# Kernel tuning notes

Measured on AMD Instinct MI355X. Metric: run time of the kernel, lower is better.

## Reference

```python
import jax, jax.numpy as jnp
import numpy as np

B, LS, LH, D1, D2 = 16, 1024, 1024, 1024, 1024


def setup_inputs() -> dict:
    key = jax.random.key(0)
    k1, k2, k3 = jax.random.split(key, 3)
    S = jax.random.normal(k1, (B, LS, D1), dtype=jnp.float32)
    H = jax.random.normal(k2, (B, LH, D2), dtype=jnp.float32)
    pad_mask = jnp.zeros((B, LS, LH), dtype=jnp.float32)  # additive mask
    W_w = jax.random.normal(k3, (D2, D1), dtype=jnp.float32) / np.sqrt(D1)
    W_b = jnp.zeros((D2,), dtype=jnp.float32)
    return {"S": S, "H": H, "pad_mask": pad_mask, "W_w": W_w, "W_b": W_b}


def reference(S, H, pad_mask, W_w, W_b):
    # Linear projection: S_ = S @ W^T + b  -> [B, LS, D2]
    S_ = jnp.einsum('bsd,ed->bse', S, W_w) + W_b
    # Unscaled dot-product scores: [B, LS, LH]
    score = jnp.einsum('bse,bte->bst', S_, H)
    score = score + pad_mask  # additive pad mask
    score = jax.nn.softmax(score, axis=-1)
    # Weighted sum of H: [B, LS, D2]
    out = jnp.einsum('bst,bte->bse', score, H)
    return out
```

## Files before the change

### kernel.cpp

```cpp
#include <hip/hip_runtime.h>
#include <stdint.h>

typedef _Float16 half8 __attribute__((ext_vector_type(8)));
typedef float floatx4 __attribute__((ext_vector_type(4)));

__device__ __forceinline__ uint16_t f16bits(_Float16 h) {
  union { _Float16 f; uint16_t u; } x; x.f = h; return x.u;
}

__device__ __forceinline__ void g2l16(const void* g, void* l) {
  __builtin_amdgcn_global_load_lds((const __attribute__((address_space(1))) void*)g,
                                   (__attribute__((address_space(3))) void*)l,
                                   16, 0, 0);
}

__global__ __launch_bounds__(256) void split_f16_kernel(
    const float* __restrict__ x, uint16_t* __restrict__ hi,
    uint16_t* __restrict__ lo, int n4) {
  int i = blockIdx.x * 256 + threadIdx.x;
  if (i >= n4) return;
  float4 v = ((const float4*)x)[i];
  ushort4 h, l;
  _Float16 a;
  a = (_Float16)v.x; h.x = f16bits(a); l.x = f16bits((_Float16)(v.x - (float)a));
  a = (_Float16)v.y; h.y = f16bits(a); l.y = f16bits((_Float16)(v.y - (float)a));
  a = (_Float16)v.z; h.z = f16bits(a); l.z = f16bits((_Float16)(v.z - (float)a));
  a = (_Float16)v.w; h.w = f16bits(a); l.w = f16bits((_Float16)(v.w - (float)a));
  ((ushort4*)hi)[i] = h;
  ((ushort4*)lo)[i] = l;
}

__global__ __launch_bounds__(256) void split_h_kernel(
    const float* __restrict__ src, uint16_t* __restrict__ hi,
    uint16_t* __restrict__ lo, uint16_t* __restrict__ ht) {
  __shared__ uint16_t tile[64][65];
  const int e0 = blockIdx.x * 64;
  const int t0 = blockIdx.y * 64;
  const size_t bb = (size_t)blockIdx.z << 20;
  const int r = threadIdx.x >> 4;
  const int c = (threadIdx.x & 15) * 4;
#pragma unroll
  for (int it = 0; it < 4; ++it) {
    const int tr = r + it * 16;
    const size_t idx = bb + (size_t)(t0 + tr) * 1024 + e0 + c;
    float4 v = *(const float4*)(src + idx);
    ushort4 h, l;
    _Float16 a;
    a = (_Float16)v.x; h.x = f16bits(a); l.x = f16bits((_Float16)(v.x - (float)a));
    a = (_Float16)v.y; h.y = f16bits(a); l.y = f16bits((_Float16)(v.y - (float)a));
    a = (_Float16)v.z; h.z = f16bits(a); l.z = f16bits((_Float16)(v.z - (float)a));
    a = (_Float16)v.w; h.w = f16bits(a); l.w = f16bits((_Float16)(v.w - (float)a));
    *(ushort4*)(hi + idx) = h;
    *(ushort4*)(lo + idx) = l;
    tile[c + 0][tr] = h.x;
    tile[c + 1][tr] = h.y;
    tile[c + 2][tr] = h.z;
    tile[c + 3][tr] = h.w;
  }
  __syncthreads();
#pragma unroll
  for (int it = 0; it < 4; ++it) {
    const int er = r + it * 16;
    ushort4 o;
    o.x = tile[er][c + 0];
    o.y = tile[er][c + 1];
    o.z = tile[er][c + 2];
    o.w = tile[er][c + 3];
    *(ushort4*)(ht + bb + (size_t)(e0 + er) * 1024 + t0 + c) = o;
  }
}

template <bool SPLIT, int MODE, int GMAP>
__global__ __launch_bounds__(512, 2) void gemm_bt(
    const uint16_t* __restrict__ Ahi, const uint16_t* __restrict__ Alo,
    const uint16_t* __restrict__ Bhi, const uint16_t* __restrict__ Blo,
    uint16_t* __restrict__ Chi, uint16_t* __restrict__ Clo,
    float* __restrict__ Cf, const float* __restrict__ mask,
    const float* __restrict__ bias, int N, int K,
    long batchA, long batchB, long batchC) {
  constexpr int NBUF = SPLIT ? 2 : 1;
  __shared__ __align__(16) uint16_t sA[2][NBUF][256 * 32];
  __shared__ __align__(16) uint16_t sB[2][NBUF][256 * 32];

  const int tid = threadIdx.x;
  const int lane = tid & 63;
  const int w = tid >> 6;
  const int wr = w >> 2, wc = w & 3;
  const int quad = lane >> 4, l16 = lane & 15;

  int m_t, n_t, z;
  if constexpr (GMAP == 0) {
    m_t = blockIdx.x; n_t = blockIdx.y; z = 0;
  } else {
    z = blockIdx.x; m_t = blockIdx.y >> 2; n_t = blockIdx.y & 3;
  }
  const int m0 = m_t * 256;
  const int n0 = n_t * 256;
  const size_t zA = (size_t)z * batchA;
  const size_t zB = (size_t)z * batchB;
  const size_t zC = (size_t)z * batchC;

  const int r0 = w * 32 + (lane >> 2);
  const int ldc = (((lane & 3) ^ ((lane >> 2) & 3)) * 16);
  const size_t rowskip = (size_t)16 * K * 2;

  const char* gAh = (const char*)(Ahi + zA + (size_t)(m0 + r0) * K) + ldc;
  const char* gBh = (const char*)(Bhi + zB + (size_t)(n0 + r0) * K) + ldc;
  const char* gAl = gAh;
  const char* gBl = gBh;
  if constexpr (SPLIT) {
    gAl = (const char*)(Alo + zA + (size_t)(m0 + r0) * K) + ldc;
    gBl = (const char*)(Blo + zB + (size_t)(n0 + r0) * K) + ldc;
  }

  auto stage = [&](int buf, int kb) {
    g2l16(gAh + kb, &sA[buf][0][(w * 32) * 32]);
    g2l16(gAh + rowskip + kb, &sA[buf][0][(w * 32 + 16) * 32]);
    g2l16(gBh + kb, &sB[buf][0][(w * 32) * 32]);
    g2l16(gBh + rowskip + kb, &sB[buf][0][(w * 32 + 16) * 32]);
    if constexpr (SPLIT) {
      g2l16(gAl + kb, &sA[buf][NBUF - 1][(w * 32) * 32]);
      g2l16(gAl + rowskip + kb, &sA[buf][NBUF - 1][(w * 32 + 16) * 32]);
      g2l16(gBl + kb, &sB[buf][NBUF - 1][(w * 32) * 32]);
      g2l16(gBl + rowskip + kb, &sB[buf][NBUF - 1][(w * 32 + 16) * 32]);
    }
  };

  const int aoff = (wr * 128 + l16) * 32 + ((quad ^ (l16 & 3)) * 8);
  const int boff = (wc * 64 + l16) * 32 + ((quad ^ (l16 & 3)) * 8);

  floatx4 acc[8][4];
  floatx4 zero = {0.f, 0.f, 0.f, 0.f};
#pragma unroll
  for (int i = 0; i < 8; ++i)
#pragma unroll
    for (int j = 0; j < 4; ++j) acc[i][j] = zero;

  const int nkt = K >> 5;
  stage(0, 0);
  __syncthreads();
  int cur = 0;
  for (int kt = 0; kt < nkt; ++kt) {
    if (kt + 1 < nkt) stage(cur ^ 1, (kt + 1) * 64);

    const uint16_t* pAh = &sA[cur][0][0];
    const uint16_t* pBh = &sB[cur][0][0];
    const uint16_t* pAl = &sA[cur][NBUF - 1][0];
    const uint16_t* pBl = &sB[cur][NBUF - 1][0];
    half8 fbh[4], fbl[4];
    if constexpr (SPLIT) {
#pragma unroll
      for (int j = 0; j < 4; ++j) fbl[j] = *(const half8*)&pBl[boff + j * 512];
    }
#pragma unroll
    for (int j = 0; j < 4; ++j) fbh[j] = *(const half8*)&pBh[boff + j * 512];
    __builtin_amdgcn_s_setprio(1);
#pragma unroll
    for (int i = 0; i < 8; ++i) {
      half8 fah = *(const half8*)&pAh[aoff + i * 512];
      if constexpr (SPLIT) {
        half8 fal = *(const half8*)&pAl[aoff + i * 512];
#pragma unroll
        for (int j = 0; j < 4; ++j)
          acc[i][j] = __builtin_amdgcn_mfma_f32_16x16x32_f16(fah, fbl[j], acc[i][j], 0, 0, 0);
#pragma unroll
        for (int j = 0; j < 4; ++j)
          acc[i][j] = __builtin_amdgcn_mfma_f32_16x16x32_f16(fah, fbh[j], acc[i][j], 0, 0, 0);
#pragma unroll
        for (int j = 0; j < 4; ++j)
          acc[i][j] = __builtin_amdgcn_mfma_f32_16x16x32_f16(fal, fbh[j], acc[i][j], 0, 0, 0);
      } else {
#pragma unroll
        for (int j = 0; j < 4; ++j)
          acc[i][j] = __builtin_amdgcn_mfma_f32_16x16x32_f16(fah, fbh[j], acc[i][j], 0, 0, 0);
      }
    }
    __builtin_amdgcn_s_setprio(0);
    __syncthreads();
    cur ^= 1;
  }

  const int crow0 = m0 + wr * 128 + quad * 4;
  const int ccol0 = n0 + wc * 64 + l16;
#pragma unroll
  for (int j = 0; j < 4; ++j) {
    const int col = ccol0 + j * 16;
    float bj = 0.f;
    if constexpr (MODE == 0) bj = bias[col];
#pragma unroll
    for (int i = 0; i < 8; ++i) {
#pragma unroll
      for (int r = 0; r < 4; ++r) {
        const int row = crow0 + i * 16 + r;
        const size_t idx = zC + (size_t)row * N + col;
        float v = acc[i][j][r];
        if constexpr (MODE == 0) {
          v += bj;
          _Float16 h = (_Float16)v;
          Chi[idx] = f16bits(h);
          Clo[idx] = f16bits((_Float16)(v - (float)h));
        } else if constexpr (MODE == 1) {
          Cf[idx] = v + mask[idx];
        } else {
          Cf[idx] = v;
        }
      }
    }
  }
}

__global__ __launch_bounds__(256) void softmax_kernel(
    const float* __restrict__ sc, uint16_t* __restrict__ p) {
  const int row = blockIdx.x;
  const float* x = sc + (size_t)row * 1024;
  const int t = threadIdx.x;
  float4 v = ((const float4*)x)[t];
  float m = fmaxf(fmaxf(v.x, v.y), fmaxf(v.z, v.w));
#pragma unroll
  for (int off = 32; off; off >>= 1) m = fmaxf(m, __shfl_xor(m, off));
  __shared__ float redm[4];
  __shared__ float reds[4];
  const int wv = t >> 6, ln = t & 63;
  if (ln == 0) redm[wv] = m;
  __syncthreads();
  m = fmaxf(fmaxf(redm[0], redm[1]), fmaxf(redm[2], redm[3]));
  float e0 = __expf(v.x - m), e1 = __expf(v.y - m);
  float e2 = __expf(v.z - m), e3 = __expf(v.w - m);
  float s = e0 + e1 + e2 + e3;
#pragma unroll
  for (int off = 32; off; off >>= 1) s += __shfl_xor(s, off);
  if (ln == 0) reds[wv] = s;
  __syncthreads();
  s = reds[0] + reds[1] + reds[2] + reds[3];
  float inv = 1.f / s;
  ushort4 o;
  o.x = f16bits((_Float16)(e0 * inv));
  o.y = f16bits((_Float16)(e1 * inv));
  o.z = f16bits((_Float16)(e2 * inv));
  o.w = f16bits((_Float16)(e3 * inv));
  ((ushort4*)(p + (size_t)row * 1024))[t] = o;
}

__global__ __launch_bounds__(256) void transpose_f16_kernel(
    const float* __restrict__ src, uint16_t* __restrict__ dst) {
  __shared__ uint16_t tile[64][65];
  const int e0 = blockIdx.x * 64;
  const int t0 = blockIdx.y * 64;
  const size_t bb = (size_t)blockIdx.z << 20;
  const int r = threadIdx.x >> 4;
  const int c = (threadIdx.x & 15) * 4;
#pragma unroll
  for (int it = 0; it < 4; ++it) {
    const int tr = r + it * 16;
    float4 v = *(const float4*)(src + bb + (size_t)(t0 + tr) * 1024 + e0 + c);
    tile[c + 0][tr] = f16bits((_Float16)v.x);
    tile[c + 1][tr] = f16bits((_Float16)v.y);
    tile[c + 2][tr] = f16bits((_Float16)v.z);
    tile[c + 3][tr] = f16bits((_Float16)v.w);
  }
  __syncthreads();
#pragma unroll
  for (int it = 0; it < 4; ++it) {
    const int er = r + it * 16;
    ushort4 o;
    o.x = tile[er][c + 0];
    o.y = tile[er][c + 1];
    o.z = tile[er][c + 2];
    o.w = tile[er][c + 3];
    *(ushort4*)(dst + bb + (size_t)(e0 + er) * 1024 + t0 + c) = o;
  }
}

extern "C" void kernel_launch(void* const* d_in, const int* in_sizes, int n_in,
                              void* d_out, int out_size, void* d_ws, size_t ws_size,
                              hipStream_t stream) {
  (void)in_sizes; (void)n_in; (void)out_size;
  const float* S    = (const float*)d_in[0];
  const float* H    = (const float*)d_in[1];
  const float* mask = (const float*)d_in[2];
  const float* Ww   = (const float*)d_in[3];
  const float* Wb   = (const float*)d_in[4];
  float* out = (float*)d_out;
  char* ws = (char*)d_ws;
  const size_t MB = 1024ull * 1024ull;

  uint16_t* Whi  = (uint16_t*)(ws + 0 * MB);
  uint16_t* Wlo  = (uint16_t*)(ws + 2 * MB);
  uint16_t* Pjhi = (uint16_t*)(ws + 4 * MB);
  uint16_t* Pjlo = (uint16_t*)(ws + 36 * MB);
  uint16_t* Hhi  = (uint16_t*)(ws + 68 * MB);
  uint16_t* Hlo  = (uint16_t*)(ws + 100 * MB);
  uint16_t* Shi  = (uint16_t*)(ws + 132 * MB);
  uint16_t* Slo  = (uint16_t*)(ws + 164 * MB);
  float*    SC   = (float*)(ws + 132 * MB);
  uint16_t* PR   = (uint16_t*)(ws + 68 * MB);

  const bool roomy = ws_size >= 229ull * MB;
  uint16_t* HT = roomy ? (uint16_t*)(ws + 196 * MB)
                       : (uint16_t*)(ws + 100 * MB);

  split_f16_kernel<<<16384, 256, 0, stream>>>(S, Shi, Slo, 4 * 1024 * 1024);
  split_f16_kernel<<<1024, 256, 0, stream>>>(Ww, Whi, Wlo, 256 * 1024);
  if (roomy) {
    split_h_kernel<<<dim3(16, 16, 16), 256, 0, stream>>>(H, Hhi, Hlo, HT);
  } else {
    split_f16_kernel<<<16384, 256, 0, stream>>>(H, Hhi, Hlo, 4 * 1024 * 1024);
  }

  gemm_bt<true, 0, 0><<<dim3(64, 4, 1), 512, 0, stream>>>(
      Shi, Slo, Whi, Wlo, Pjhi, Pjlo, nullptr, nullptr, Wb,
      1024, 1024, 0, 0, 0);
  gemm_bt<true, 1, 1><<<dim3(16, 16, 1), 512, 0, stream>>>(
      Pjhi, Pjlo, Hhi, Hlo, nullptr, nullptr, SC, mask, nullptr,
      1024, 1024, 1048576, 1048576, 1048576);
  softmax_kernel<<<16384, 256, 0, stream>>>(SC, PR);
  if (!roomy) {
    transpose_f16_kernel<<<dim3(16, 16, 16), 256, 0, stream>>>(H, HT);
  }
  gemm_bt<false, 2, 1><<<dim3(16, 16, 1), 512, 0, stream>>>(
      PR, nullptr, HT, nullptr, nullptr, nullptr, out, nullptr, nullptr,
      1024, 1024, 1048576, 1048576, 1048576);
}
```

Before: 556.4 us.

## Replace double-buffered GEMM staging with five-slot half-tile LDS ring pipeline

Replaces the two-stage LDS double buffer in the split-f16 GEMM with a five-slot ring of half-tile units. Loads are issued deeper ahead, interleaved across four sub-phases of the MFMA loop, and guarded by explicit vmcnt waits and raw s_barriers instead of a full __syncthreads per k-step. The aim is to hide global-to-LDS latency and spread barrier stalls. In exchange it adds more LDS per block, which may reduce occupancy, more barriers per iteration, and hand-tuned waitcnt logic that is fragile.

```diff
diff --git a/kernel.cpp b/kernel.cpp
--- a/kernel.cpp
+++ b/kernel.cpp
@@ -78,9 +78,11 @@
     float* __restrict__ Cf, const float* __restrict__ mask,
     const float* __restrict__ bias, int N, int K,
     long batchA, long batchB, long batchC) {
-  constexpr int NBUF = SPLIT ? 2 : 1;
-  __shared__ __align__(16) uint16_t sA[2][NBUF][256 * 32];
-  __shared__ __align__(16) uint16_t sB[2][NBUF][256 * 32];
+  constexpr int UNIT = SPLIT ? 16384 : 8192;
+  constexpr int OAL = 4096;
+  constexpr int OBH = SPLIT ? 8192 : 4096;
+  constexpr int OBL = 12288;
+  __shared__ __align__(16) uint16_t lds[5 * UNIT];
 
   const int tid = threadIdx.x;
   const int lane = tid & 63;
@@ -100,34 +102,31 @@
   const size_t zB = (size_t)z * batchB;
   const size_t zC = (size_t)z * batchC;
 
-  const int r0 = w * 32 + (lane >> 2);
+  const int r4 = w * 16 + (lane >> 2);
   const int ldc = (((lane & 3) ^ ((lane >> 2) & 3)) * 16);
-  const size_t rowskip = (size_t)16 * K * 2;
-
-  const char* gAh = (const char*)(Ahi + zA + (size_t)(m0 + r0) * K) + ldc;
-  const char* gBh = (const char*)(Bhi + zB + (size_t)(n0 + r0) * K) + ldc;
+  const size_t halfskip = (size_t)128 * K * 2;
+
+  const char* gAh = (const char*)(Ahi + zA + (size_t)(m0 + r4) * K) + ldc;
+  const char* gBh = (const char*)(Bhi + zB + (size_t)(n0 + r4) * K) + ldc;
   const char* gAl = gAh;
   const char* gBl = gBh;
   if constexpr (SPLIT) {
-    gAl = (const char*)(Alo + zA + (size_t)(m0 + r0) * K) + ldc;
-    gBl = (const char*)(Blo + zB + (size_t)(n0 + r0) * K) + ldc;
-  }
-
-  auto stage = [&](int buf, int kb) {
-    g2l16(gAh + kb, &sA[buf][0][(w * 32) * 32]);
-    g2l16(gAh + rowskip + kb, &sA[buf][0][(w * 32 + 16) * 32]);
-    g2l16(gBh + kb, &sB[buf][0][(w * 32) * 32]);
-    g2l16(gBh + rowskip + kb, &sB[buf][0][(w * 32 + 16) * 32]);
-    if constexpr (SPLIT) {
-      g2l16(gAl + kb, &sA[buf][NBUF - 1][(w * 32) * 32]);
-      g2l16(gAl + rowskip + kb, &sA[buf][NBUF - 1][(w * 32 + 16) * 32]);
-      g2l16(gBl + kb, &sB[buf][NBUF - 1][(w * 32) * 32]);
-      g2l16(gBl + rowskip + kb, &sB[buf][NBUF - 1][(w * 32 + 16) * 32]);
-    }
+    gAl = (const char*)(Alo + zA + (size_t)(m0 + r4) * K) + ldc;
+    gBl = (const char*)(Blo + zB + (size_t)(n0 + r4) * K) + ldc;
+  }
+
+  auto issue_unit = [&](int u, int sl) {
+    const int tt = u >> 1;
+    const size_t go = (size_t)(u & 1) * halfskip + (size_t)tt * 64;
+    uint16_t* ub = &lds[sl * UNIT] + w * 512;
+    g2l16(gAh + go, ub);
+    if constexpr (SPLIT) g2l16(gAl + go, ub + OAL);
+    g2l16(gBh + go, ub + OBH);
+    if constexpr (SPLIT) g2l16(gBl + go, ub + OBL);
   };
 
-  const int aoff = (wr * 128 + l16) * 32 + ((quad ^ (l16 & 3)) * 8);
-  const int boff = (wc * 64 + l16) * 32 + ((quad ^ (l16 & 3)) * 8);
+  const int aoff = l16 * 32 + ((quad ^ (l16 & 3)) * 8);
+  const int boff = ((wc & 1) * 64 + l16) * 32 + ((quad ^ (l16 & 3)) * 8);
 
   floatx4 acc[8][4];
   floatx4 zero = {0.f, 0.f, 0.f, 0.f};
@@ -137,47 +136,89 @@
     for (int j = 0; j < 4; ++j) acc[i][j] = zero;
 
   const int nkt = K >> 5;
-  stage(0, 0);
-  __syncthreads();
-  int cur = 0;
-  for (int kt = 0; kt < nkt; ++kt) {
-    if (kt + 1 < nkt) stage(cur ^ 1, (kt + 1) * 64);
-
-    const uint16_t* pAh = &sA[cur][0][0];
-    const uint16_t* pBh = &sB[cur][0][0];
-    const uint16_t* pAl = &sA[cur][NBUF - 1][0];
-    const uint16_t* pBl = &sB[cur][NBUF - 1][0];
+  const int NU = nkt * 2;
+
+  issue_unit(0, 0);
+  issue_unit(1, 1);
+  issue_unit(2, 2);
+  if constexpr (SPLIT)
+    asm volatile("s_waitcnt vmcnt(4)" ::: "memory");
+  else
+    asm volatile("s_waitcnt vmcnt(2)" ::: "memory");
+  __builtin_amdgcn_s_barrier();
+  asm volatile("" ::: "memory");
+
+  int sl0 = 0;
+  for (int t = 0; t < nkt; ++t) {
+    const int sl1 = (sl0 + 1 == 5) ? 0 : sl0 + 1;
+    const int si0 = (sl0 + 3 >= 5) ? sl0 - 2 : sl0 + 3;
+    const int si1 = (sl0 + 4 >= 5) ? sl0 - 1 : sl0 + 4;
+    const uint16_t* uA = &lds[(wr ? sl1 : sl0) * UNIT];
+    const uint16_t* uB = &lds[((wc >> 1) ? sl1 : sl0) * UNIT];
     half8 fbh[4], fbl[4];
-    if constexpr (SPLIT) {
-#pragma unroll
-      for (int j = 0; j < 4; ++j) fbl[j] = *(const half8*)&pBl[boff + j * 512];
+#pragma unroll
+    for (int p = 0; p < 4; ++p) {
+      half8 fah[2], fal[2];
+      if (p == 0) {
+        if constexpr (SPLIT) {
+#pragma unroll
+          for (int j = 0; j < 4; ++j)
+            fbl[j] = *(const half8*)&uB[OBL + boff + j * 512];
+        }
+#pragma unroll
+        for (int j = 0; j < 4; ++j)
+          fbh[j] = *(const half8*)&uB[OBH + boff + j * 512];
+      }
+      fah[0] = *(const half8*)&uA[aoff + (2 * p) * 512];
+      fah[1] = *(const half8*)&uA[aoff + (2 * p + 1) * 512];
+      if constexpr (SPLIT) {
+        fal[0] = *(const half8*)&uA[OAL + aoff + (2 * p) * 512];
+        fal[1] = *(const half8*)&uA[OAL + aoff + (2 * p + 1) * 512];
+      }
+      if (p == 0 && 2 * t + 3 < NU) issue_unit(2 * t + 3, si0);
+      if (p == 2 && 2 * t + 4 < NU) issue_unit(2 * t + 4, si1);
+      asm volatile("" ::: "memory");
+      __builtin_amdgcn_s_barrier();
+      asm volatile("s_waitcnt lgkmcnt(0)" ::: "memory");
+      __builtin_amdgcn_sched_barrier(0);
+      __builtin_amdgcn_s_setprio(1);
+#pragma unroll
+      for (int ii = 0; ii < 2; ++ii) {
+        const int i = 2 * p + ii;
+        if constexpr (SPLIT) {
+#pragma unroll
+          for (int j = 0; j < 4; ++j)
+            acc[i][j] = __builtin_amdgcn_mfma_f32_16x16x32_f16(fah[ii], fbl[j], acc[i][j], 0, 0, 0);
+#pragma unroll
+          for (int j = 0; j < 4; ++j)
+            acc[i][j] = __builtin_amdgcn_mfma_f32_16x16x32_f16(fah[ii], fbh[j], acc[i][j], 0, 0, 0);
+#pragma unroll
+          for (int j = 0; j < 4; ++j)
+            acc[i][j] = __builtin_amdgcn_mfma_f32_16x16x32_f16(fal[ii], fbh[j], acc[i][j], 0, 0, 0);
+        } else {
+#pragma unroll
+          for (int j = 0; j < 4; ++j)
+            acc[i][j] = __builtin_amdgcn_mfma_f32_16x16x32_f16(fah[ii], fbh[j], acc[i][j], 0, 0, 0);
+        }
+      }
+      __builtin_amdgcn_s_setprio(0);
+      if (p < 3) {
+        asm volatile("" ::: "memory");
+        __builtin_amdgcn_s_barrier();
+      }
     }
-#pragma unroll
-    for (int j = 0; j < 4; ++j) fbh[j] = *(const half8*)&pBh[boff + j * 512];
-    __builtin_amdgcn_s_setprio(1);
-#pragma unroll
-    for (int i = 0; i < 8; ++i) {
-      half8 fah = *(const half8*)&pAh[aoff + i * 512];
-      if constexpr (SPLIT) {
-        half8 fal = *(const half8*)&pAl[aoff + i * 512];
-#pragma unroll
-        for (int j = 0; j < 4; ++j)
-          acc[i][j] = __builtin_amdgcn_mfma_f32_16x16x32_f16(fah, fbl[j], acc[i][j], 0, 0, 0);
-#pragma unroll
-        for (int j = 0; j < 4; ++j)
-          acc[i][j] = __builtin_amdgcn_mfma_f32_16x16x32_f16(fah, fbh[j], acc[i][j], 0, 0, 0);
-#pragma unroll
-        for (int j = 0; j < 4; ++j)
-          acc[i][j] = __builtin_amdgcn_mfma_f32_16x16x32_f16(fal, fbh[j], acc[i][j], 0, 0, 0);
-      } else {
-#pragma unroll
-        for (int j = 0; j < 4; ++j)
-          acc[i][j] = __builtin_amdgcn_mfma_f32_16x16x32_f16(fah, fbh[j], acc[i][j], 0, 0, 0);
-      }
+    if (t + 2 < nkt) {
+      if constexpr (SPLIT)
+        asm volatile("s_waitcnt vmcnt(4)" ::: "memory");
+      else
+        asm volatile("s_waitcnt vmcnt(2)" ::: "memory");
+    } else if (t + 1 < nkt) {
+      asm volatile("s_waitcnt vmcnt(0)" ::: "memory");
     }
-    __builtin_amdgcn_s_setprio(0);
-    __syncthreads();
-    cur ^= 1;
+    asm volatile("" ::: "memory");
+    __builtin_amdgcn_s_barrier();
+    asm volatile("" ::: "memory");
+    sl0 = (sl0 + 2 >= 5) ? sl0 - 3 : sl0 + 2;
   }
 
   const int crow0 = m0 + wr * 128 + quad * 4;
```

Result: faster. 538.8 us (-3.2%).
